# Kernel optimization log

Measured on AMD Instinct MI355X. Metric: run time of the kernel, lower is better.

## Reference

```python
import jax, jax.numpy as jnp
import numpy as np

NEG_BIG = -9e15  # matches torch's -9000000000000000.0 mask value


def setup_inputs() -> dict:
    key = jax.random.key(0)
    k1, k2, k3, k4 = jax.random.split(key, 4)
    B, N, Din, Dout = 4, 4096, 256, 128
    x = jax.random.normal(k1, (B, N, Din), dtype=jnp.float32)
    adj = jax.random.randint(k2, (B, N, N), 0, 2, dtype=jnp.int32)
    weight = jax.random.normal(k3, (Din, Dout), dtype=jnp.float32) * (1.414 * (6.0 / (Din + Dout)) ** 0.5)
    a = jax.random.normal(k4, (2 * Dout, 1), dtype=jnp.float32) * 0.1
    bias = jnp.zeros((Dout,), dtype=jnp.float32)
    return {"x": x, "adj": adj, "weight": weight, "a": a, "bias": bias}


def reference(x, adj, weight, a, bias):
    Dout = weight.shape[1]
    h = jnp.matmul(x, weight)                       # [B, N, Dout]
    Wh1 = jnp.matmul(h, a[:Dout, :])                # [B, N, 1]
    Wh2 = jnp.matmul(h, a[Dout:, :])                # [B, N, 1]
    e = jax.nn.gelu(Wh1 + jnp.swapaxes(Wh2, 1, 2), approximate=False)  # [B, N, N]
    attention = jnp.where(adj > 0, e, NEG_BIG)
    attention = jax.nn.softmax(attention, axis=1)   # softmax over dim=1, as in torch code
    out = jnp.matmul(attention, h)                  # [B, N, Dout]
    out = jax.nn.gelu(out, approximate=False)
    # F.normalize(p=2, dim=1): L2-normalize over the node dimension
    norm = jnp.sqrt(jnp.sum(out * out, axis=1, keepdims=True))
    out = out / jnp.maximum(norm, 1e-12)
    return out + bias
```

## Files before the change

### kernel.cpp

```cpp
#include <hip/hip_runtime.h>
#include <hip/hip_bf16.h>
#include <stdint.h>


#define NN   4096
#define BB   4
#define DIN  256
#define DOUT 128

typedef unsigned short u16;
typedef _Float16 f16x8 __attribute__((ext_vector_type(8)));
typedef __attribute__((ext_vector_type(4))) float f32x4;

__device__ __forceinline__ u16 f2h_bits(float f) {
  _Float16 h = (_Float16)f;
  union { _Float16 h; u16 u; } v; v.h = h;
  return v.u;
}

__device__ __forceinline__ float erf_f(float x) {
  float ax = __builtin_fabsf(x);
  float t  = __builtin_amdgcn_rcpf(__builtin_fmaf(0.3275911f, ax, 1.0f));
  float p  = __builtin_fmaf(1.061405429f, t, -1.453152027f);
  p = __builtin_fmaf(p, t, 1.421413741f);
  p = __builtin_fmaf(p, t, -0.284496736f);
  p = __builtin_fmaf(p, t, 0.254829592f);
  p = p * t;
  float e  = __expf(-ax * ax);
  float er = __builtin_fmaf(-p, e, 1.0f);
  return copysignf(er, x);
}

__device__ __forceinline__ float gelu_f(float z) {
  float hz = 0.5f * z;
  return __builtin_fmaf(hz, erf_f(z * 0.70710678118654752f), hz);
}

__device__ __forceinline__ float exp_gelu(float z) { return __expf(gelu_f(z)); }

__global__ __launch_bounds__(256, 2) void k1_proj(
    const float* __restrict__ x, const float* __restrict__ weight,
    const float* __restrict__ a, u16* __restrict__ hT,
    float* __restrict__ Wh1, float* __restrict__ Wh2)
{
  __shared__ float xs[32 * 256];
  __shared__ float T[128 * 33];
  __shared__ float P2a[8 * 32], P2b[8 * 32];

  const int b = blockIdx.y, n0 = blockIdx.x * 32;
  const int tid = threadIdx.x;

  const float4* xsrc = (const float4*)(x + ((size_t)b * NN + n0) * DIN);
  float4* xd = (float4*)xs;
#pragma unroll
  for (int v = 0; v < 8; ++v) xd[tid + v * 256] = xsrc[tid + v * 256];
  __syncthreads();

  const int dg = tid & 31, rg = tid >> 5;
  float acc[4][4] = {};
  const float4* W4 = (const float4*)weight;
#pragma unroll 4
  for (int k = 0; k < 256; ++k) {
    float4 wr = W4[k * 32 + dg];
#pragma unroll
    for (int rr = 0; rr < 4; ++rr) {
      float xv = xs[(rg * 4 + rr) * 256 + k];
      acc[rr][0] = fmaf(xv, wr.x, acc[rr][0]);
      acc[rr][1] = fmaf(xv, wr.y, acc[rr][1]);
      acc[rr][2] = fmaf(xv, wr.z, acc[rr][2]);
      acc[rr][3] = fmaf(xv, wr.w, acc[rr][3]);
    }
  }
#pragma unroll
  for (int rr = 0; rr < 4; ++rr)
#pragma unroll
    for (int dd = 0; dd < 4; ++dd)
      T[(dg * 4 + dd) * 33 + rg * 4 + rr] = acc[rr][dd];
  __syncthreads();

  {
    const int d = tid & 127, half = tid >> 7;
    unsigned int uu[8];
#pragma unroll
    for (int p = 0; p < 8; ++p) {
      float f0 = T[d * 33 + half * 16 + p * 2];
      float f1 = T[d * 33 + half * 16 + p * 2 + 1];
      uu[p] = (unsigned int)f2h_bits(f0) | ((unsigned int)f2h_bits(f1) << 16);
    }
    u16* dst = hT + ((size_t)b * DOUT + d) * NN + n0 + half * 16;
    ((uint4*)dst)[0] = make_uint4(uu[0], uu[1], uu[2], uu[3]);
    ((uint4*)dst)[1] = make_uint4(uu[4], uu[5], uu[6], uu[7]);
  }
  {
    const int r = tid & 31, g8 = tid >> 5;
    float p1 = 0.f, p2 = 0.f;
#pragma unroll
    for (int q = 0; q < 16; ++q) {
      int d = g8 * 16 + q;
      float hv = T[d * 33 + r];
      p1 = fmaf(hv, a[d], p1);
      p2 = fmaf(hv, a[DOUT + d], p2);
    }
    P2a[g8 * 32 + r] = p1;
    P2b[g8 * 32 + r] = p2;
  }
  __syncthreads();
  if (tid < 32) {
    float s1 = 0.f, s2 = 0.f;
#pragma unroll
    for (int g8 = 0; g8 < 8; ++g8) { s1 += P2a[g8 * 32 + tid]; s2 += P2b[g8 * 32 + tid]; }
    Wh1[b * NN + n0 + tid] = s1;
    Wh2[b * NN + n0 + tid] = s2;
  }
}

__global__ __launch_bounds__(256) void k2_fused(
    const int* __restrict__ adj, const float* __restrict__ Wh1,
    const float* __restrict__ Wh2, float* __restrict__ S,
    unsigned int* __restrict__ m32)
{
  const int b = blockIdx.z, jt = blockIdx.x, ic = blockIdx.y;
  const int tid = threadIdx.x;
  const int j = jt * 256 + tid;
  const int lane = tid & 63;
  const int jg = jt * 4 + (tid >> 6);
  const int i0 = ic * 128;

  const float wh2 = Wh2[b * NN + j];
  const int* ap = adj + ((size_t)b * NN + i0) * NN + j;
  const float* w1p = Wh1 + b * NN + i0;
  unsigned int* mlo = m32 + ((size_t)b * 128 + jg * 2) * NN + i0;
  unsigned int* mhi = mlo + NN;

  float s = 0.f;
  for (int g = 0; g < 2; ++g) {
    unsigned long long acc64 = 0ull;
#pragma unroll
    for (int gg = 0; gg < 4; ++gg) {
      int av[16]; float w1v[16];
#pragma unroll
      for (int k = 0; k < 16; ++k) {
        const int ii = g * 64 + gg * 16 + k;
        av[k]  = ap[(size_t)ii * NN];
        w1v[k] = w1p[ii];
      }
#pragma unroll
      for (int k = 0; k < 16; ++k) {
        const unsigned long long bal = __ballot(av[k] > 0);
        if (lane == gg * 16 + k) acc64 = bal;
        const float E = exp_gelu(w1v[k] + wh2);
        s += (av[k] > 0) ? E : 0.f;
      }
    }
    mlo[g * 64 + lane] = (unsigned int)acc64;
    mhi[g * 64 + lane] = (unsigned int)(acc64 >> 32);
  }
  atomicAdd(&S[b * NN + j], s);
}

__global__ __launch_bounds__(256) void k25_rcp(const float* __restrict__ S,
                                               float* __restrict__ Sinv)
{
  int id = blockIdx.x * 256 + threadIdx.x;
  Sinv[id] = 1.0f / S[id];
}

__global__ __launch_bounds__(256, 2) void k3_attn(
    const unsigned int* __restrict__ m32, const float* __restrict__ Wh1,
    const float* __restrict__ Wh2, const float* __restrict__ Sinv,
    const u16* __restrict__ hT, float* __restrict__ out,
    float* __restrict__ norm2)
{
  __shared__ __align__(16) u16 buf[4][128 * 32];

  const int b = blockIdx.y;
  const int i0 = blockIdx.x * 32;
  const int tid = threadIdx.x;
  const int w = tid >> 6, lane = tid & 63;
  const int m = lane & 15, quad = lane >> 4;

  const float w1a = Wh1[b * NN + i0 + m];
  const float w1b = Wh1[b * NN + i0 + 16 + m];
  const unsigned int* mbase = m32 + (size_t)b * 128 * NN;
  const u16* hTb = hT + (size_t)b * DOUT * NN;
  const u16* srcbase = hTb + (size_t)(lane >> 2) * NN + (lane & 3) * 8;

  f32x4 acc0[8], acc1[8];
#pragma unroll
  for (int t = 0; t < 8; ++t) {
    acc0[t] = (f32x4){0.f, 0.f, 0.f, 0.f};
    acc1[t] = (f32x4){0.f, 0.f, 0.f, 0.f};
  }

  for (int c = 0; c < 32; ++c) {
    const int j0 = w * 1024 + c * 32;
    const int jw = j0 >> 5;

    __builtin_amdgcn_s_waitcnt(0xC07F);
#pragma unroll
    for (int inst = 0; inst < 8; ++inst) {
      const u16* g = srcbase + (size_t)inst * 16 * NN + j0;
      __builtin_amdgcn_global_load_lds(
          (const __attribute__((address_space(1))) void*)g,
          (__attribute__((address_space(3))) void*)&buf[w][inst * 512],
          16, 0, 0);
    }

    const unsigned int Ma = mbase[(size_t)jw * NN + i0 + m];
    const unsigned int Mb = mbase[(size_t)jw * NN + i0 + 16 + m];
    const unsigned int mba = (Ma >> (quad * 8)) & 0xFFu;
    const unsigned int mbb = (Mb >> (quad * 8)) & 0xFFu;

    const int jq = j0 + quad * 8;
    const float4* wp = (const float4*)(Wh2 + b * NN + jq);
    float4 w2a = wp[0], w2b = wp[1];
    const float4* sp = (const float4*)(Sinv + b * NN + jq);
    float4 sva = sp[0], svb = sp[1];

    f16x8 ah_a, ah_b;
    ah_a[0] = (_Float16)((mba & 1u)   ? exp_gelu(w1a + w2a.x) * sva.x : 0.f);
    ah_a[1] = (_Float16)((mba & 2u)   ? exp_gelu(w1a + w2a.y) * sva.y : 0.f);
    ah_a[2] = (_Float16)((mba & 4u)   ? exp_gelu(w1a + w2a.z) * sva.z : 0.f);
    ah_a[3] = (_Float16)((mba & 8u)   ? exp_gelu(w1a + w2a.w) * sva.w : 0.f);
    ah_a[4] = (_Float16)((mba & 16u)  ? exp_gelu(w1a + w2b.x) * svb.x : 0.f);
    ah_a[5] = (_Float16)((mba & 32u)  ? exp_gelu(w1a + w2b.y) * svb.y : 0.f);
    ah_a[6] = (_Float16)((mba & 64u)  ? exp_gelu(w1a + w2b.z) * svb.z : 0.f);
    ah_a[7] = (_Float16)((mba & 128u) ? exp_gelu(w1a + w2b.w) * svb.w : 0.f);
    ah_b[0] = (_Float16)((mbb & 1u)   ? exp_gelu(w1b + w2a.x) * sva.x : 0.f);
    ah_b[1] = (_Float16)((mbb & 2u)   ? exp_gelu(w1b + w2a.y) * sva.y : 0.f);
    ah_b[2] = (_Float16)((mbb & 4u)   ? exp_gelu(w1b + w2a.z) * sva.z : 0.f);
    ah_b[3] = (_Float16)((mbb & 8u)   ? exp_gelu(w1b + w2a.w) * sva.w : 0.f);
    ah_b[4] = (_Float16)((mbb & 16u)  ? exp_gelu(w1b + w2b.x) * svb.x : 0.f);
    ah_b[5] = (_Float16)((mbb & 32u)  ? exp_gelu(w1b + w2b.y) * svb.y : 0.f);
    ah_b[6] = (_Float16)((mbb & 64u)  ? exp_gelu(w1b + w2b.z) * svb.z : 0.f);
    ah_b[7] = (_Float16)((mbb & 128u) ? exp_gelu(w1b + w2b.w) * svb.w : 0.f);

    __builtin_amdgcn_s_waitcnt(0x0F70);

#pragma unroll
    for (int t = 0; t < 8; ++t) {
      f16x8 bf = *(const f16x8*)&buf[w][(t * 16 + m) * 32 + quad * 8];
      acc0[t] = __builtin_amdgcn_mfma_f32_16x16x32_f16(ah_a, bf, acc0[t], 0, 0, 0);
      acc1[t] = __builtin_amdgcn_mfma_f32_16x16x32_f16(ah_b, bf, acc1[t], 0, 0, 0);
    }
  }

  float* red = (float*)&buf[0][0];
  float p2[2] = {0.f, 0.f};
#pragma unroll
  for (int rt = 0; rt < 2; ++rt) {
    __syncthreads();
#pragma unroll
    for (int t = 0; t < 8; ++t)
#pragma unroll
      for (int r = 0; r < 4; ++r)
        red[w * 2048 + (t * 4 + r) * 64 + lane] = rt ? acc1[t][r] : acc0[t][r];
    __syncthreads();
#pragma unroll
    for (int tt = 0; tt < 2; ++tt) {
      const int t = w * 2 + tt;
#pragma unroll
      for (int r = 0; r < 4; ++r) {
        const int o = (t * 4 + r) * 64 + lane;
        float v = red[o] + red[2048 + o] + red[4096 + o] + red[6144 + o];
        float gv = gelu_f(v);
        out[((size_t)b * NN + i0 + rt * 16 + quad * 4 + r) * DOUT + t * 16 + m] = gv;
        p2[tt] = fmaf(gv, gv, p2[tt]);
      }
    }
  }
#pragma unroll
  for (int tt = 0; tt < 2; ++tt) {
    float ps = p2[tt];
    ps += __shfl_xor(ps, 16);
    ps += __shfl_xor(ps, 32);
    if (quad == 0)
      atomicAdd(&norm2[b * DOUT + (w * 2 + tt) * 16 + m], ps);
  }
}

__global__ __launch_bounds__(256) void k4b_scale(
    float* __restrict__ out, const float* __restrict__ norm2,
    const float* __restrict__ bias)
{
  int id = blockIdx.x * 256 + threadIdx.x;
  int d = id & 127;
  int b = id >> 19;
  float nrm = sqrtf(norm2[b * DOUT + d]);
  float sc = 1.0f / fmaxf(nrm, 1e-12f);
  out[id] = fmaf(out[id], sc, bias[d]);
}

extern "C" void kernel_launch(void* const* d_in, const int* in_sizes, int n_in,
                              void* d_out, int out_size, void* d_ws, size_t ws_size,
                              hipStream_t stream)
{
  const float* x      = (const float*)d_in[0];
  const int*   adj    = (const int*)d_in[1];
  const float* weight = (const float*)d_in[2];
  const float* a      = (const float*)d_in[3];
  const float* bias   = (const float*)d_in[4];
  float* out = (float*)d_out;

  char* ws = (char*)d_ws;
  u16*   hT     = (u16*)ws;
  float* Wh1    = (float*)(ws + (size_t)4 * 1024 * 1024);
  float* Wh2    = Wh1 + BB * NN;
  float* S      = Wh2 + BB * NN;
  float* Sinv   = S + BB * NN;
  unsigned int* m32 = (unsigned int*)(Sinv + BB * NN);
  float* norm2  = (float*)((char*)m32 + (size_t)BB * 128 * NN * 4);

  hipMemsetAsync(S, 0, (size_t)BB * NN * sizeof(float), stream);
  hipMemsetAsync(norm2, 0, (size_t)BB * DOUT * sizeof(float), stream);

  k1_proj<<<dim3(NN / 32, BB), 256, 0, stream>>>(x, weight, a, hT, Wh1, Wh2);
  k2_fused<<<dim3(16, 32, BB), 256, 0, stream>>>(adj, Wh1, Wh2, S, m32);
  k25_rcp<<<dim3(BB * NN / 256), 256, 0, stream>>>(S, Sinv);
  k3_attn<<<dim3(NN / 32, BB), 256, 0, stream>>>(m32, Wh1, Wh2, Sinv, hT, out, norm2);
  k4b_scale<<<dim3((BB * NN * DOUT) / 256), 256, 0, stream>>>(out, norm2, bias);
}
```

Before: 507.7 us.

## Double-buffer LDS tiles and prefetch mask/Wh2/Sinv in attention kernel

The attention kernel now splits each wave's LDS tile into two buffers. While the current 32-column chunk is being consumed by MFMA, the hT tile for the next chunk is loaded with global_load_lds into the other buffer. The mask word, Wh2 and Sinv values for the next chunk are also loaded into registers one iteration ahead. The wait after the score computation now lets only the just-issued prefetch loads stay outstanding, so global latency overlaps with exp/GELU and MFMA work. In exchange, LDS per block doubles, register pressure rises, and the last iteration issues a redundant prefetch.

```diff
diff --git a/kernel.cpp b/kernel.cpp
--- a/kernel.cpp
+++ b/kernel.cpp
@@ -171,7 +171,7 @@
     const u16* __restrict__ hT, float* __restrict__ out,
     float* __restrict__ norm2)
 {
-  __shared__ __align__(16) u16 buf[4][128 * 32];
+  __shared__ __align__(16) u16 buf[4][2][4096];
 
   const int b = blockIdx.y;
   const int i0 = blockIdx.x * 32;
@@ -192,30 +192,57 @@
     acc1[t] = (f32x4){0.f, 0.f, 0.f, 0.f};
   }
 
+  const int jbase = w * 1024;
+
+  unsigned int Ma, Mb;
+  float4 w2a, w2b, sva, svb;
+  {
+    const int j0 = jbase;
+    const int jw = j0 >> 5;
+    Ma = mbase[(size_t)jw * NN + i0 + m];
+    Mb = mbase[(size_t)jw * NN + i0 + 16 + m];
+    const int jq = j0 + quad * 8;
+    const float4* wp = (const float4*)(Wh2 + b * NN + jq);
+    w2a = wp[0]; w2b = wp[1];
+    const float4* sp = (const float4*)(Sinv + b * NN + jq);
+    sva = sp[0]; svb = sp[1];
+  }
+#pragma unroll
+  for (int inst = 0; inst < 8; ++inst) {
+    const u16* g = srcbase + (size_t)inst * 16 * NN + jbase;
+    __builtin_amdgcn_global_load_lds(
+        (const __attribute__((address_space(1))) void*)g,
+        (__attribute__((address_space(3))) void*)&buf[w][0][inst * 512],
+        16, 0, 0);
+  }
+
   for (int c = 0; c < 32; ++c) {
-    const int j0 = w * 1024 + c * 32;
-    const int jw = j0 >> 5;
+    const int cur = c & 1;
+    const int cn = (c < 31) ? c + 1 : 31;
+    const int j0n = jbase + cn * 32;
+
+    const int jwn = j0n >> 5;
+    const unsigned int Ma_n = mbase[(size_t)jwn * NN + i0 + m];
+    const unsigned int Mb_n = mbase[(size_t)jwn * NN + i0 + 16 + m];
+    const int jqn = j0n + quad * 8;
+    const float4* wpn = (const float4*)(Wh2 + b * NN + jqn);
+    const float4 w2a_n = wpn[0], w2b_n = wpn[1];
+    const float4* spn = (const float4*)(Sinv + b * NN + jqn);
+    const float4 sva_n = spn[0], svb_n = spn[1];
 
     __builtin_amdgcn_s_waitcnt(0xC07F);
+    __builtin_amdgcn_sched_barrier(0);
 #pragma unroll
     for (int inst = 0; inst < 8; ++inst) {
-      const u16* g = srcbase + (size_t)inst * 16 * NN + j0;
+      const u16* g = srcbase + (size_t)inst * 16 * NN + j0n;
       __builtin_amdgcn_global_load_lds(
           (const __attribute__((address_space(1))) void*)g,
-          (__attribute__((address_space(3))) void*)&buf[w][inst * 512],
+          (__attribute__((address_space(3))) void*)&buf[w][cur ^ 1][inst * 512],
           16, 0, 0);
     }
 
-    const unsigned int Ma = mbase[(size_t)jw * NN + i0 + m];
-    const unsigned int Mb = mbase[(size_t)jw * NN + i0 + 16 + m];
     const unsigned int mba = (Ma >> (quad * 8)) & 0xFFu;
     const unsigned int mbb = (Mb >> (quad * 8)) & 0xFFu;
-
-    const int jq = j0 + quad * 8;
-    const float4* wp = (const float4*)(Wh2 + b * NN + jq);
-    float4 w2a = wp[0], w2b = wp[1];
-    const float4* sp = (const float4*)(Sinv + b * NN + jq);
-    float4 sva = sp[0], svb = sp[1];
 
     f16x8 ah_a, ah_b;
     ah_a[0] = (_Float16)((mba & 1u)   ? exp_gelu(w1a + w2a.x) * sva.x : 0.f);
@@ -235,17 +262,22 @@
     ah_b[6] = (_Float16)((mbb & 64u)  ? exp_gelu(w1b + w2b.z) * svb.z : 0.f);
     ah_b[7] = (_Float16)((mbb & 128u) ? exp_gelu(w1b + w2b.w) * svb.w : 0.f);
 
-    __builtin_amdgcn_s_waitcnt(0x0F70);
+    __builtin_amdgcn_sched_barrier(0);
+    __builtin_amdgcn_s_waitcnt(0x0F78);
+    __builtin_amdgcn_sched_barrier(0);
 
 #pragma unroll
     for (int t = 0; t < 8; ++t) {
-      f16x8 bf = *(const f16x8*)&buf[w][(t * 16 + m) * 32 + quad * 8];
+      f16x8 bf = *(const f16x8*)&buf[w][cur][(t * 16 + m) * 32 + quad * 8];
       acc0[t] = __builtin_amdgcn_mfma_f32_16x16x32_f16(ah_a, bf, acc0[t], 0, 0, 0);
       acc1[t] = __builtin_amdgcn_mfma_f32_16x16x32_f16(ah_b, bf, acc1[t], 0, 0, 0);
     }
-  }
-
-  float* red = (float*)&buf[0][0];
+
+    Ma = Ma_n; Mb = Mb_n;
+    w2a = w2a_n; w2b = w2b_n; sva = sva_n; svb = svb_n;
+  }
+
+  float* red = (float*)&buf[0][0][0];
   float p2[2] = {0.f, 0.f};
 #pragma unroll
   for (int rt = 0; rt < 2; ++rt) {
```

Result: no change. 501.9 us (-1.1%).
